# Optimization experiments

Hardware: AMD Instinct MI355X
Metric: run time of the kernel (lower is better)

## Reference

```python
import jax, jax.numpy as jnp
import numpy as np

B, T, C = 2, 2048, 1024
H, M = 16, 64
D = C // H  # head_dim = 64


def setup_inputs() -> dict:
    key = jax.random.key(0)
    ks = jax.random.split(key, 6)
    x = jax.random.normal(ks[0], (B, T, C), dtype=jnp.float32)
    Wqkv = jax.random.normal(ks[1], (3 * C, C), dtype=jnp.float32) / np.sqrt(C)
    bqkv = jax.random.normal(ks[2], (3 * C,), dtype=jnp.float32) * 0.02
    Wout = jax.random.normal(ks[3], (C, C), dtype=jnp.float32) / np.sqrt(C)
    bout = jax.random.normal(ks[4], (C,), dtype=jnp.float32) * 0.02
    proj = jax.random.normal(ks[5], (H, D, M), dtype=jnp.float32) / np.sqrt(D)
    return {"x": x, "Wqkv": Wqkv, "bqkv": bqkv, "Wout": Wout, "bout": bout, "proj": proj}


def reference(x, Wqkv, bqkv, Wout, bout, proj):
    b, t, c = x.shape
    h, d, m = proj.shape
    qkv = x @ Wqkv.T + bqkv                          # [B,T,3C]
    q, k, v = jnp.split(qkv, 3, axis=-1)
    # [B,T,C] -> [B,H,T,D]
    to_heads = lambda z: z.reshape(b, t, h, d).transpose(0, 2, 1, 3)
    q, k, v = to_heads(q), to_heads(k), to_heads(v)
    qf, kf, vf = q.astype(jnp.float32), k.astype(jnp.float32), v.astype(jnp.float32)
    pf = proj.astype(jnp.float32)
    q_prime = jax.nn.relu(jnp.einsum('bhtd,hdm->bhtm', qf, pf))
    k_prime = jax.nn.relu(jnp.einsum('bhtd,hdm->bhtm', kf, pf))
    k_cumsum = jnp.cumsum(k_prime, axis=2)                        # [B,H,T,M]
    kv_prod = jnp.einsum('bhtm,bhtd->bhtmd', k_prime, vf)          # [B,H,T,M,D]
    kv_cumsum = jnp.cumsum(kv_prod, axis=2)                        # [B,H,T,M,D]
    context = jnp.einsum('bhtm,bhtmd->bhtd', q_prime, kv_cumsum)   # [B,H,T,D]
    norm = jnp.einsum('bhtm,bhtm->bht', q_prime, k_cumsum)         # [B,H,T]
    out = context / (norm[..., None] + 1e-6)
    out = out.astype(x.dtype).transpose(0, 2, 1, 3).reshape(b, t, c)
    return out @ Wout.T + bout
```

## Files before the change

### kernel.cpp

```cpp
#include <hip/hip_runtime.h>
#include <cstddef>

#define B_  2
#define T_  2048
#define C_  1024
#define H_  16
#define D_  64
#define M_  64
#define NC_ 32
#define CH_ 64

typedef __attribute__((ext_vector_type(8))) short bf16x8;
typedef __attribute__((ext_vector_type(4))) float f32x4;

__device__ __forceinline__ ushort f2bf(float f) {
    union { float f; unsigned u; } v; v.f = f;
    unsigned r = v.u + 0x7FFF + ((v.u >> 16) & 1);
    return (ushort)(r >> 16);
}
__device__ __forceinline__ float bf2f(ushort u) {
    union { unsigned u; float f; } x; x.u = ((unsigned)u) << 16; return x.f;
}

__device__ __forceinline__ void gld_lds16(const ushort* g, ushort* lds) {
    __builtin_amdgcn_global_load_lds(
        (const __attribute__((address_space(1))) unsigned int*)g,
        (__attribute__((address_space(3))) unsigned int*)lds,
        16, 0, 0);
}

__device__ __forceinline__ bf16x8 frag_ld(const ushort* lds, int row16, int k0, int lane) {
    int r = row16 + (lane & 15);
    int byte = ((k0 * 2) + ((lane >> 4) << 4)) ^ ((r & 7) << 4);
    return *(const bf16x8*)((const char*)lds + r * 128 + byte);
}

#define VMCNT(n) asm volatile("s_waitcnt vmcnt(" #n ")" ::: "memory")
#define BAR() do { __builtin_amdgcn_s_barrier(); __builtin_amdgcn_sched_barrier(0); } while (0)

#define SEG1_ 256
#define SEG2_ 512
#define SEG3_ 1536
#define SEG4_ 1792
#define NPREP_ 1804

__global__ __launch_bounds__(256) void prep_all(
    const float* __restrict__ x, const float* __restrict__ Wqkv,
    const float* __restrict__ bqkv, const float* __restrict__ Wout,
    const float* __restrict__ proj,
    ushort* __restrict__ Wbt, ushort* __restrict__ xbf,
    ushort* __restrict__ WoutBf, float* __restrict__ bbig)
{
    __shared__ float Ws[64 * 128];
    __shared__ float Ps[64 * 64];
    const int blk = blockIdx.x, t = threadIdx.x;
    if (blk < SEG1_) {
        const int sel = blk >> 7, h = (blk >> 3) & 15, cc = blk & 7;
        const int rowbase = sel * 1024 + h * 64;
        {
            const int r0 = t >> 5, cq = t & 31;
#pragma unroll
            for (int k = 0; k < 8; ++k) {
                int r = r0 + 8 * k;
                *(float4*)&Ws[r * 128 + cq * 4] =
                    *(const float4*)&Wqkv[(size_t)(rowbase + r) * 1024 + cc * 128 + cq * 4];
            }
        }
#pragma unroll
        for (int k = 0; k < 4; ++k) {
            int i4 = t + 256 * k;
            *(float4*)&Ps[i4 * 4] = *(const float4*)&proj[h * 4096 + i4 * 4];
        }
        __syncthreads();
#pragma unroll
        for (int k = 0; k < 2; ++k) {
            int id = t + 256 * k;
            int m4 = id >> 5, c4 = id & 31;
            float4 a0 = {0.f,0.f,0.f,0.f}, a1 = a0, a2 = a0, a3 = a0;
            for (int d = 0; d < 64; ++d) {
                float4 w = *(const float4*)&Ws[d * 128 + c4 * 4];
                float4 p = *(const float4*)&Ps[d * 64 + m4 * 4];
                a0.x += p.x*w.x; a0.y += p.x*w.y; a0.z += p.x*w.z; a0.w += p.x*w.w;
                a1.x += p.y*w.x; a1.y += p.y*w.y; a1.z += p.y*w.z; a1.w += p.y*w.w;
                a2.x += p.z*w.x; a2.y += p.z*w.y; a2.z += p.z*w.z; a2.w += p.z*w.w;
                a3.x += p.w*w.x; a3.y += p.w*w.y; a3.z += p.w*w.z; a3.w += p.w*w.w;
            }
            size_t obase = (size_t)(rowbase + m4 * 4) * 1024 + cc * 128 + c4 * 4;
            ushort4 o0 = { f2bf(a0.x), f2bf(a0.y), f2bf(a0.z), f2bf(a0.w) };
            ushort4 o1 = { f2bf(a1.x), f2bf(a1.y), f2bf(a1.z), f2bf(a1.w) };
            ushort4 o2 = { f2bf(a2.x), f2bf(a2.y), f2bf(a2.z), f2bf(a2.w) };
            ushort4 o3 = { f2bf(a3.x), f2bf(a3.y), f2bf(a3.z), f2bf(a3.w) };
            *(ushort4*)&Wbt[obase]          = o0;
            *(ushort4*)&Wbt[obase + 1024]   = o1;
            *(ushort4*)&Wbt[obase + 2048]   = o2;
            *(ushort4*)&Wbt[obase + 3072]   = o3;
        }
    } else if (blk < SEG2_) {
        int bo = blk - SEG1_;
#pragma unroll
        for (int pass = 0; pass < 4; ++pass) {
            int i4 = bo * 1024 + pass * 256 + t;
            float4 v = ((const float4*)Wqkv)[524288 + i4];
            ushort4 o = { f2bf(v.x), f2bf(v.y), f2bf(v.z), f2bf(v.w) };
            ((ushort4*)(Wbt + 2097152))[i4] = o;
        }
    } else if (blk < SEG3_) {
        int bo = blk - SEG2_;
#pragma unroll
        for (int pass = 0; pass < 4; ++pass) {
            int i4 = bo * 1024 + pass * 256 + t;
            float4 v = ((const float4*)x)[i4];
            ushort4 o = { f2bf(v.x), f2bf(v.y), f2bf(v.z), f2bf(v.w) };
            ((ushort4*)xbf)[i4] = o;
        }
    } else if (blk < SEG4_) {
        int bo = blk - SEG3_;
#pragma unroll
        for (int pass = 0; pass < 4; ++pass) {
            int i4 = bo * 1024 + pass * 256 + t;
            float4 v = ((const float4*)Wout)[i4];
            ushort4 o = { f2bf(v.x), f2bf(v.y), f2bf(v.z), f2bf(v.w) };
            ((ushort4*)WoutBf)[i4] = o;
        }
    } else {
        int j = (blk - SEG4_) * 256 + t;
        if (j < 2048) {
            int sel = j >> 10, hm = j & 1023, h = hm >> 6, m = hm & 63;
            const float* b = bqkv + sel * C_ + h * D_;
            const float* p = proj + (size_t)h * D_ * M_ + m;
            float acc = 0.f;
#pragma unroll 8
            for (int d = 0; d < D_; ++d) acc += b[d] * p[(size_t)d * M_];
            bbig[j] = acc;
        } else {
            bbig[j] = bqkv[j];
        }
    }
}

__device__ __forceinline__ void stage_G0(const ushort* __restrict__ Ag, const ushort* __restrict__ Bg,
                                         ushort* Abuf, ushort* Bbuf,
                                         int m0, int n0, int K, int kcol, int w, int lane) {
    const int l8 = lane >> 3, lc = (lane & 7) * 8;
#pragma unroll
    for (int i = 0; i < 4; ++i) {
        int c = w * 4 + i;
        if (c < 8) {
            int fr = (c < 4) ? c * 8 : 64 + (c - 4) * 8;
            int r = fr + l8;
            int cs = lc ^ ((r & 7) << 3);
            gld_lds16(Ag + (size_t)(m0 + r) * K + kcol + cs, Abuf + fr * 64);
        } else {
            int cb = c - 8, g = cb / 6, k8 = cb - g * 6;
            int fr = g * 96 + k8 * 8;
            int r = fr + l8;
            int cs = lc ^ ((r & 7) << 3);
            gld_lds16(Bg + (size_t)(n0 + r) * K + kcol + cs, Bbuf + fr * 64);
        }
    }
}

__device__ __forceinline__ void stage_G1(const ushort* __restrict__ Ag, const ushort* __restrict__ Bg,
                                         ushort* Abuf, ushort* Bbuf,
                                         int m0, int n0, int K, int kcol, int w, int lane) {
    const int l8 = lane >> 3, lc = (lane & 7) * 8;
#pragma unroll
    for (int i = 0; i < 3; ++i) {
        int cb = w * 3 + i, g = cb / 6, k8 = cb - g * 6;
        int fr = g * 96 + 48 + k8 * 8;
        int r = fr + l8;
        int cs = lc ^ ((r & 7) << 3);
        gld_lds16(Bg + (size_t)(n0 + r) * K + kcol + cs, Bbuf + fr * 64);
    }
    {
        int fr = (w < 4) ? 32 + w * 8 : 96 + (w - 4) * 8;
        int r = fr + l8;
        int cs = lc ^ ((r & 7) << 3);
        gld_lds16(Ag + (size_t)(m0 + r) * K + kcol + cs, Abuf + fr * 64);
    }
}

__device__ __forceinline__ void phase_mfma(const ushort* Abuf, const ushort* Bbuf,
                                           f32x4 (&acc)[4][6], int wr, int wc, int lane,
                                           int Mh, int Nh) {
    bf16x8 a[2][2], b[3][2];
#pragma unroll
    for (int i = 0; i < 2; ++i)
#pragma unroll
        for (int ks = 0; ks < 2; ++ks)
            a[i][ks] = frag_ld(Abuf, wr + Mh * 32 + i * 16, ks * 32, lane);
#pragma unroll
    for (int j = 0; j < 3; ++j)
#pragma unroll
        for (int ks = 0; ks < 2; ++ks)
            b[j][ks] = frag_ld(Bbuf, wc + Nh * 48 + j * 16, ks * 32, lane);
    __builtin_amdgcn_s_setprio(1);
#pragma unroll
    for (int ks = 0; ks < 2; ++ks)
#pragma unroll
        for (int i = 0; i < 2; ++i)
#pragma unroll
            for (int j = 0; j < 3; ++j)
                acc[Mh * 2 + i][Nh * 3 + j] = __builtin_amdgcn_mfma_f32_16x16x32_bf16(
                    a[i][ks], b[j][ks], acc[Mh * 2 + i][Nh * 3 + j], 0, 0, 0);
    __builtin_amdgcn_s_setprio(0);
}

__global__ __launch_bounds__(512) void gemm_8phase(
    const ushort* __restrict__ A,
    const ushort* __restrict__ Bt,
    const float* __restrict__ bias,
    ushort* __restrict__ Cout,
    int M, int N, int K, int reluLimit)
{
    __shared__ __align__(16) ushort lds[65536];

    const int tid = threadIdx.x, w = tid >> 6, lane = tid & 63;
    const int m0 = blockIdx.y * 128, n0 = blockIdx.x * 384;
    const int wr = (w >> 2) * 64, wc = (w & 3) * 96;
    f32x4 acc[4][6] = {};
    const int NT = K / 64;

    stage_G0(A, Bt, lds, lds + 16384, m0, n0, K, 0, w, lane);
    stage_G1(A, Bt, lds, lds + 16384, m0, n0, K, 0, w, lane);

    for (int kt = 0; kt < NT - 1; ++kt) {
        const int p = kt & 1;
        ushort* Acur = lds + p * 8192;
        ushort* Anxt = lds + (p ^ 1) * 8192;
        ushort* Bcur = lds + 16384 + p * 24576;
        ushort* Bnxt = lds + 16384 + (p ^ 1) * 24576;
        const int kc1 = (kt + 1) * 64;
        VMCNT(4); BAR();
        stage_G0(A, Bt, Anxt, Bnxt, m0, n0, K, kc1, w, lane);
        phase_mfma(Acur, Bcur, acc, wr, wc, lane, 0, 0);
        VMCNT(5); BAR();
        phase_mfma(Acur, Bcur, acc, wr, wc, lane, 0, 1);
        VMCNT(4); BAR();
        stage_G1(A, Bt, Anxt, Bnxt, m0, n0, K, kc1, w, lane);
        phase_mfma(Acur, Bcur, acc, wr, wc, lane, 1, 0);
        phase_mfma(Acur, Bcur, acc, wr, wc, lane, 1, 1);
    }
    {
        const int p = (NT - 1) & 1;
        ushort* Acur = lds + p * 8192;
        ushort* Bcur = lds + 16384 + p * 24576;
        VMCNT(4); BAR();
        phase_mfma(Acur, Bcur, acc, wr, wc, lane, 0, 0);
        VMCNT(1); BAR();
        phase_mfma(Acur, Bcur, acc, wr, wc, lane, 0, 1);
        VMCNT(0); BAR();
        phase_mfma(Acur, Bcur, acc, wr, wc, lane, 1, 0);
        phase_mfma(Acur, Bcur, acc, wr, wc, lane, 1, 1);
    }

    const int crow = (lane >> 4) * 4, ccol = lane & 15;
#pragma unroll
    for (int nj = 0; nj < 6; ++nj) {
        int col = n0 + wc + nj * 16 + ccol;
        float bv = bias[col];
        bool rl = col < reluLimit;
#pragma unroll
        for (int mi = 0; mi < 4; ++mi) {
#pragma unroll
            for (int rr = 0; rr < 4; ++rr) {
                int row = m0 + wr + mi * 16 + crow + rr;
                float v = acc[mi][nj][rr] + bv;
                if (rl) v = fmaxf(v, 0.f);
                Cout[(size_t)row * N + col] = f2bf(v);
            }
        }
    }
}

__global__ __launch_bounds__(256, 2) void gemm_mfma_bt(
    const ushort* __restrict__ A, const ushort* __restrict__ Bt,
    const float* __restrict__ bias, float* __restrict__ Cmat,
    int M, int N, int K, int reluLimit)
{
    __shared__ __align__(16) ushort As[128 * 32];
    __shared__ __align__(16) ushort Bs[128 * 32];
    const int tid  = threadIdx.x;
    const int wave = tid >> 6, lane = tid & 63;
    const int m0 = blockIdx.y * 128, n0 = blockIdx.x * 128;
    const int wr = (wave >> 1) * 64, wc = (wave & 1) * 64;
    f32x4 acc[4][4] = {};

    const int lrow = lane >> 2;
    const int lcol = (lane & 3) * 8;
    ushort* AsB0 = &As[(wave * 2 + 0) * 512];
    ushort* AsB1 = &As[(wave * 2 + 1) * 512];
    ushort* BsB0 = &Bs[(wave * 2 + 0) * 512];
    ushort* BsB1 = &Bs[(wave * 2 + 1) * 512];
    const ushort* Ag0 = A  + (size_t)(m0 + wave * 32 + lrow) * K + lcol;
    const ushort* Ag1 = Ag0 + (size_t)16 * K;
    const ushort* Bg0 = Bt + (size_t)(n0 + wave * 32 + lrow) * K + lcol;
    const ushort* Bg1 = Bg0 + (size_t)16 * K;

    const int frow = lane & 15, fk = (lane >> 4) * 8;

    for (int k0 = 0; k0 < K; k0 += 32) {
        __syncthreads();
        gld_lds16(Ag0 + k0, AsB0);
        gld_lds16(Ag1 + k0, AsB1);
        gld_lds16(Bg0 + k0, BsB0);
        gld_lds16(Bg1 + k0, BsB1);
        __syncthreads();
        bf16x8 af[4], bfr[4];
#pragma unroll
        for (int i = 0; i < 4; ++i)
            af[i] = *(const bf16x8*)&As[(wr + i * 16 + frow) * 32 + fk];
#pragma unroll
        for (int j = 0; j < 4; ++j)
            bfr[j] = *(const bf16x8*)&Bs[(wc + j * 16 + frow) * 32 + fk];
#pragma unroll
        for (int i = 0; i < 4; ++i)
#pragma unroll
            for (int j = 0; j < 4; ++j)
                acc[i][j] = __builtin_amdgcn_mfma_f32_16x16x32_bf16(af[i], bfr[j], acc[i][j], 0, 0, 0);
    }

    const int crow = (lane >> 4) * 4, ccol = lane & 15;
#pragma unroll
    for (int j = 0; j < 4; ++j) {
        int col = n0 + wc + j * 16 + ccol;
        float bv = bias[col];
        bool rl = col < reluLimit;
#pragma unroll
        for (int i = 0; i < 4; ++i) {
#pragma unroll
            for (int r = 0; r < 4; ++r) {
                int row = m0 + wr + i * 16 + crow + r;
                float v = acc[i][j][r] + bv;
                if (rl) v = fmaxf(v, 0.f);
                Cmat[(size_t)row * N + col] = v;
            }
        }
    }
}

__global__ __launch_bounds__(256) void chunk_kv_mfma(
    const ushort* __restrict__ out1, ushort* __restrict__ VtG,
    float* __restrict__ St, float* __restrict__ sks)
{
    __shared__ unsigned Tl[64 * 76];
    __shared__ ushort Ktb[64 * 64];
    __shared__ ushort Vtb[64 * 64];
    __shared__ float skp[4][64];
    const int blk = blockIdx.x, c = blk & 31, bh = blk >> 5;
    const int b = bh >> 4, h = bh & 15, t0 = c * CH_;
    const int tid = threadIdx.x, wave = tid >> 6, lane = tid & 63;
    const ushort* kg = out1 + (size_t)(b * T_ + t0) * 3072 + C_ + h * D_;
    const ushort* vg = kg + C_;

#pragma unroll
    for (int it = 0; it < 2; ++it) {
        int i = tid + it * 256, r = i >> 3, sl = i & 7;
        bf16x8 v = *(const bf16x8*)(kg + (size_t)r * 3072 + sl * 8);
        unsigned* dst = &Tl[r * 76 + sl * 8];
        uint4 w0 = { (ushort)v[0], (ushort)v[1], (ushort)v[2], (ushort)v[3] };
        uint4 w1 = { (ushort)v[4], (ushort)v[5], (ushort)v[6], (ushort)v[7] };
        *(uint4*)dst = w0;
        *(uint4*)(dst + 4) = w1;
    }
    __syncthreads();
    {
        int m = tid >> 2, tc = tid & 3;
        bf16x8 va, vb;
        float s = 0.f;
#pragma unroll
        for (int k = 0; k < 8; ++k) {
            ushort u = (ushort)Tl[(tc * 16 + k) * 76 + m];
            va[k] = (short)u; s += bf2f(u);
        }
#pragma unroll
        for (int k = 0; k < 8; ++k) {
            ushort u = (ushort)Tl[(tc * 16 + 8 + k) * 76 + m];
            vb[k] = (short)u; s += bf2f(u);
        }
        skp[tc][m] = s;
        int b0 = (tc * 32) ^ ((m & 7) << 4);
        int b1 = (tc * 32 + 16) ^ ((m & 7) << 4);
        *(bf16x8*)((char*)Ktb + m * 128 + b0) = va;
        *(bf16x8*)((char*)Ktb + m * 128 + b1) = vb;
    }
    __syncthreads();
#pragma unroll
    for (int it = 0; it < 2; ++it) {
        int i = tid + it * 256, r = i >> 3, sl = i & 7;
        bf16x8 v = *(const bf16x8*)(vg + (size_t)r * 3072 + sl * 8);
        unsigned* dst = &Tl[r * 76 + sl * 8];
        uint4 w0 = { (ushort)v[0], (ushort)v[1], (ushort)v[2], (ushort)v[3] };
        uint4 w1 = { (ushort)v[4], (ushort)v[5], (ushort)v[6], (ushort)v[7] };
        *(uint4*)dst = w0;
        *(uint4*)(dst + 4) = w1;
    }
    __syncthreads();
    {
        int d = tid >> 2, tc = tid & 3;
        bf16x8 va, vb;
#pragma unroll
        for (int k = 0; k < 8; ++k) va[k] = (short)(ushort)Tl[(tc * 16 + k) * 76 + d];
#pragma unroll
        for (int k = 0; k < 8; ++k) vb[k] = (short)(ushort)Tl[(tc * 16 + 8 + k) * 76 + d];
        int b0 = (tc * 32) ^ ((d & 7) << 4);
        int b1 = (tc * 32 + 16) ^ ((d & 7) << 4);
        *(bf16x8*)((char*)Vtb + d * 128 + b0) = va;
        *(bf16x8*)((char*)Vtb + d * 128 + b1) = vb;
        ushort* og = VtG + (size_t)blk * 4096 + d * 64 + tc * 16;
        *(bf16x8*)og = va;
        *(bf16x8*)(og + 8) = vb;
    }
    __syncthreads();
    const int wr = wave * 16, g = lane >> 4, ccol = lane & 15;
    f32x4 acc[4] = {};
#pragma unroll
    for (int k0 = 0; k0 < 64; k0 += 32) {
        bf16x8 av = frag_ld(Vtb, wr, k0, lane);
#pragma unroll
        for (int j = 0; j < 4; ++j)
            acc[j] = __builtin_amdgcn_mfma_f32_16x16x32_bf16(av, frag_ld(Ktb, j * 16, k0, lane), acc[j], 0, 0, 0);
    }
    float* stg = St + (size_t)blk * 4096;
#pragma unroll
    for (int j = 0; j < 4; ++j)
#pragma unroll
        for (int r = 0; r < 4; ++r)
            stg[(wr + g * 4 + r) * 64 + j * 16 + ccol] = acc[j][r];
    if (tid < 64)
        sks[(size_t)blk * 64 + tid] = skp[0][tid] + skp[1][tid] + skp[2][tid] + skp[3][tid];
}

__global__ __launch_bounds__(256) void chunk_scan2(const float* __restrict__ St,
                                                   const float* __restrict__ sks,
                                                   ushort* __restrict__ Sbf,
                                                   ushort* __restrict__ skb) {
    if (blockIdx.x < 512) {
        int id = blockIdx.x * 256 + threadIdx.x;
        int bh = id >> 12, e = id & 4095;
        const float* p = St + (size_t)bh * NC_ * 4096 + e;
        ushort* q = Sbf + (size_t)bh * NC_ * 4096 + e;
        float run = 0.f;
        for (int c = 0; c < NC_; ++c) {
            q[(size_t)c * 4096] = f2bf(run);
            run += p[(size_t)c * 4096];
        }
    } else {
        int id2 = (blockIdx.x - 512) * 256 + threadIdx.x;
        int bh = id2 >> 6, m = id2 & 63;
        const float* p = sks + (size_t)bh * NC_ * 64 + m;
        ushort* q = skb + (size_t)bh * NC_ * 64 + m;
        float run = 0.f;
        for (int c = 0; c < NC_; ++c) {
            q[c * 64] = f2bf(run);
            run += p[c * 64];
        }
    }
}

__global__ __launch_bounds__(256) void chunk_attn_mfma(
    const ushort* __restrict__ out1, const ushort* __restrict__ VtG,
    const ushort* __restrict__ Sbf, const ushort* __restrict__ skb,
    ushort* __restrict__ attnBf)
{
    __shared__ ushort Ql[64 * 64];
    __shared__ ushort Kl[64 * 64];
    __shared__ ushort Vl[64 * 64];
    __shared__ ushort Al[64 * 64];
    __shared__ ushort Sl[80 * 64];
    const int blk = blockIdx.x, c = blk & 31, bh = blk >> 5;
    const int b = bh >> 4, h = bh & 15, t0 = c * CH_;
    const int tid = threadIdx.x, wave = tid >> 6, lane = tid & 63;
    const ushort* qg  = out1 + (size_t)(b * T_ + t0) * 3072 + h * D_;
    const ushort* kg  = qg + C_;
    const ushort* vtg = VtG + (size_t)blk * 4096;
    const ushort* sbg = Sbf + (size_t)blk * 4096;
#pragma unroll
    for (int it = 0; it < 2; ++it) {
        int i = tid + it * 256, r = i >> 3, sl = i & 7;
        int lo = (sl * 16) ^ ((r & 7) << 4);
        *(bf16x8*)((char*)Ql + r * 128 + lo) = *(const bf16x8*)(qg + (size_t)r * 3072 + sl * 8);
        *(bf16x8*)((char*)Kl + r * 128 + lo) = *(const bf16x8*)(kg + (size_t)r * 3072 + sl * 8);
        *(bf16x8*)((char*)Vl + r * 128 + lo) = *(const bf16x8*)(vtg + r * 64 + sl * 8);
        *(bf16x8*)((char*)Sl + r * 128 + lo) = *(const bf16x8*)(sbg + r * 64 + sl * 8);
    }
    if (tid < 8)
        *(bf16x8*)((char*)Sl + 64 * 128 + tid * 16) = *(const bf16x8*)(skb + (size_t)blk * 64 + tid * 8);
    __syncthreads();

    const int wr = wave * 16, g = lane >> 4, ccol = lane & 15;
    f32x4 accA[4] = {};
#pragma unroll
    for (int k0 = 0; k0 < 64; k0 += 32) {
        bf16x8 aq = frag_ld(Ql, wr, k0, lane);
#pragma unroll
        for (int j = 0; j < 4; ++j)
            accA[j] = __builtin_amdgcn_mfma_f32_16x16x32_bf16(aq, frag_ld(Kl, j * 16, k0, lane), accA[j], 0, 0, 0);
    }
    float rsum[4] = {0.f, 0.f, 0.f, 0.f};
#pragma unroll
    for (int j = 0; j < 4; ++j) {
#pragma unroll
        for (int r = 0; r < 4; ++r) {
            int tl = wr + g * 4 + r, sl2 = j * 16 + ccol;
            float v = (sl2 <= tl) ? accA[j][r] : 0.f;
            rsum[r] += v;
            *(ushort*)((char*)Al + tl * 128 + ((sl2 * 2) ^ ((tl & 7) << 4))) = f2bf(v);
        }
    }
#pragma unroll
    for (int r = 0; r < 4; ++r) {
        rsum[r] += __shfl_xor(rsum[r], 1);
        rsum[r] += __shfl_xor(rsum[r], 2);
        rsum[r] += __shfl_xor(rsum[r], 4);
        rsum[r] += __shfl_xor(rsum[r], 8);
    }
    f32x4 accC[4] = {};
    f32x4 accE = {};
#pragma unroll
    for (int k0 = 0; k0 < 64; k0 += 32) {
        bf16x8 aa = frag_ld(Al, wr, k0, lane);
#pragma unroll
        for (int j = 0; j < 4; ++j)
            accC[j] = __builtin_amdgcn_mfma_f32_16x16x32_bf16(aa, frag_ld(Vl, j * 16, k0, lane), accC[j], 0, 0, 0);
    }
#pragma unroll
    for (int k0 = 0; k0 < 64; k0 += 32) {
        bf16x8 aq = frag_ld(Ql, wr, k0, lane);
#pragma unroll
        for (int j = 0; j < 4; ++j)
            accC[j] = __builtin_amdgcn_mfma_f32_16x16x32_bf16(aq, frag_ld(Sl, j * 16, k0, lane), accC[j], 0, 0, 0);
        accE = __builtin_amdgcn_mfma_f32_16x16x32_bf16(aq, frag_ld(Sl, 64, k0, lane), accE, 0, 0, 0);
    }
    ushort* og = attnBf + (size_t)(b * T_ + t0) * C_ + h * D_;
#pragma unroll
    for (int r = 0; r < 4; ++r) {
        float nq = __shfl(accE[r], (lane & 48));
        float inv = 1.f / (nq + rsum[r] + 1e-6f);
        int tl = wr + g * 4 + r;
#pragma unroll
        for (int j = 0; j < 4; ++j)
            og[(size_t)tl * C_ + j * 16 + ccol] = f2bf(accC[j][r] * inv);
    }
}

extern "C" void kernel_launch(void* const* d_in, const int* in_sizes, int n_in,
                              void* d_out, int out_size, void* d_ws, size_t ws_size,
                              hipStream_t stream) {
    (void)in_sizes; (void)n_in; (void)out_size; (void)ws_size;
    const float* x    = (const float*)d_in[0];
    const float* Wqkv = (const float*)d_in[1];
    const float* bqkv = (const float*)d_in[2];
    const float* Wout = (const float*)d_in[3];
    const float* bout = (const float*)d_in[4];
    const float* proj = (const float*)d_in[5];
    float* out = (float*)d_out;
    char* ws = (char*)d_ws;

    ushort* Wbt    = (ushort*)(ws);
    ushort* xbf    = (ushort*)(ws + (6ull  << 20));
    ushort* WoutBf = (ushort*)(ws + (14ull << 20));
    ushort* attnBf = (ushort*)(ws + (16ull << 20));
    float*  bbig   = (float*) (ws + (24ull << 20));
    ushort* out1   = (ushort*)(ws + (25ull << 20));
    ushort* VtG    = (ushort*)(ws + (49ull << 20));
    float*  St     = (float*) (ws + (57ull << 20));
    ushort* Sbf    = (ushort*)(ws + (73ull << 20));
    float*  sks    = (float*) (ws + (81ull << 20));
    ushort* skb    = (ushort*)(ws + (82ull << 20));

    prep_all<<<NPREP_, 256, 0, stream>>>(x, Wqkv, bqkv, Wout, proj,
                                         Wbt, xbf, WoutBf, bbig);
    gemm_8phase<<<dim3(8, 32), 512, 0, stream>>>(xbf, Wbt, bbig, out1,
                                                 4096, 3072, 1024, 2048);
    chunk_kv_mfma<<<1024, 256, 0, stream>>>(out1, VtG, St, sks);
    chunk_scan2<<<520, 256, 0, stream>>>(St, sks, Sbf, skb);
    chunk_attn_mfma<<<1024, 256, 0, stream>>>(out1, VtG, Sbf, skb, attnBf);
    gemm_mfma_bt<<<dim3(8, 32), 256, 0, stream>>>(attnBf, WoutBf, bout, out,
                                                  4096, 1024, 1024, 0);
}
```

Before: 99.63 us.

## Pipeline output GEMM with 8-phase double-buffered kernel and store chunk states in bf16

Replaces the simple single-buffered output-projection GEMM with a 512-thread, double-buffered, swizzled-LDS, phase-interleaved kernel modeled on the QKV GEMM, so global loads overlap MFMA work. Separately, per-chunk KV state matrices are written as bf16 instead of fp32, which halves the traffic into the scan kernel. The bf16 state storage adds rounding error before the prefix sum, which accumulates over the 32 chunks.

```diff
diff --git a/kernel.cpp b/kernel.cpp
--- a/kernel.cpp
+++ b/kernel.cpp
@@ -207,10 +207,8 @@
 }
 
 __global__ __launch_bounds__(512) void gemm_8phase(
-    const ushort* __restrict__ A,
-    const ushort* __restrict__ Bt,
-    const float* __restrict__ bias,
-    ushort* __restrict__ Cout,
+    const ushort* __restrict__ A, const ushort* __restrict__ Bt,
+    const float* __restrict__ bias, ushort* __restrict__ Cout,
     int M, int N, int K, int reluLimit)
 {
     __shared__ __align__(16) ushort lds[65536];
@@ -273,67 +271,121 @@
     }
 }
 
-__global__ __launch_bounds__(256, 2) void gemm_mfma_bt(
+__device__ __forceinline__ void g2_stage_G0(const ushort* __restrict__ Ag, const ushort* __restrict__ Bg,
+                                            ushort* Abuf, ushort* Bbuf,
+                                            int m0, int n0, int K, int kcol, int w, int lane) {
+    const int l8 = lane >> 3, lc = (lane & 7) * 8;
+    {
+        int rbase = (w < 4) ? w * 8 : 64 + (w - 4) * 8;
+        int r = rbase + l8;
+        int cs = lc ^ ((r & 7) << 3);
+        gld_lds16(Ag + (size_t)(m0 + r) * K + kcol + cs, Abuf + rbase * 64);
+    }
+    {
+        int rbase = (w >> 1) * 32 + (w & 1) * 8;
+        int r = rbase + l8;
+        int cs = lc ^ ((r & 7) << 3);
+        gld_lds16(Bg + (size_t)(n0 + r) * K + kcol + cs, Bbuf + rbase * 64);
+    }
+}
+
+__device__ __forceinline__ void g2_stage_G1(const ushort* __restrict__ Ag, const ushort* __restrict__ Bg,
+                                            ushort* Abuf, ushort* Bbuf,
+                                            int m0, int n0, int K, int kcol, int w, int lane) {
+    const int l8 = lane >> 3, lc = (lane & 7) * 8;
+    {
+        int rbase = 16 + (w >> 1) * 32 + (w & 1) * 8;
+        int r = rbase + l8;
+        int cs = lc ^ ((r & 7) << 3);
+        gld_lds16(Bg + (size_t)(n0 + r) * K + kcol + cs, Bbuf + rbase * 64);
+    }
+    {
+        int rbase = (w < 4) ? 32 + w * 8 : 96 + (w - 4) * 8;
+        int r = rbase + l8;
+        int cs = lc ^ ((r & 7) << 3);
+        gld_lds16(Ag + (size_t)(m0 + r) * K + kcol + cs, Abuf + rbase * 64);
+    }
+}
+
+__device__ __forceinline__ void g2_phase(const ushort* Abuf, const ushort* Bbuf,
+                                         f32x4 (&acc)[4][2], int wr, int wc, int lane,
+                                         int Mh, int Nh) {
+    bf16x8 a[2][2], b[2];
+#pragma unroll
+    for (int i = 0; i < 2; ++i)
+#pragma unroll
+        for (int ks = 0; ks < 2; ++ks)
+            a[i][ks] = frag_ld(Abuf, wr + Mh * 32 + i * 16, ks * 32, lane);
+#pragma unroll
+    for (int ks = 0; ks < 2; ++ks)
+        b[ks] = frag_ld(Bbuf, wc + Nh * 16, ks * 32, lane);
+    __builtin_amdgcn_s_setprio(1);
+#pragma unroll
+    for (int ks = 0; ks < 2; ++ks)
+#pragma unroll
+        for (int i = 0; i < 2; ++i)
+            acc[Mh * 2 + i][Nh] = __builtin_amdgcn_mfma_f32_16x16x32_bf16(
+                a[i][ks], b[ks], acc[Mh * 2 + i][Nh], 0, 0, 0);
+    __builtin_amdgcn_s_setprio(0);
+}
+
+__global__ __launch_bounds__(512, 4) void gemm2_8phase(
     const ushort* __restrict__ A, const ushort* __restrict__ Bt,
-    const float* __restrict__ bias, float* __restrict__ Cmat,
-    int M, int N, int K, int reluLimit)
+    const float* __restrict__ bias, float* __restrict__ Cout,
+    int M, int N, int K)
 {
-    __shared__ __align__(16) ushort As[128 * 32];
-    __shared__ __align__(16) ushort Bs[128 * 32];
-    const int tid  = threadIdx.x;
-    const int wave = tid >> 6, lane = tid & 63;
+    __shared__ __align__(16) ushort lds[32768];
+
+    const int tid = threadIdx.x, w = tid >> 6, lane = tid & 63;
     const int m0 = blockIdx.y * 128, n0 = blockIdx.x * 128;
-    const int wr = (wave >> 1) * 64, wc = (wave & 1) * 64;
-    f32x4 acc[4][4] = {};
-
-    const int lrow = lane >> 2;
-    const int lcol = (lane & 3) * 8;
-    ushort* AsB0 = &As[(wave * 2 + 0) * 512];
-    ushort* AsB1 = &As[(wave * 2 + 1) * 512];
-    ushort* BsB0 = &Bs[(wave * 2 + 0) * 512];
-    ushort* BsB1 = &Bs[(wave * 2 + 1) * 512];
-    const ushort* Ag0 = A  + (size_t)(m0 + wave * 32 + lrow) * K + lcol;
-    const ushort* Ag1 = Ag0 + (size_t)16 * K;
-    const ushort* Bg0 = Bt + (size_t)(n0 + wave * 32 + lrow) * K + lcol;
-    const ushort* Bg1 = Bg0 + (size_t)16 * K;
-
-    const int frow = lane & 15, fk = (lane >> 4) * 8;
-
-    for (int k0 = 0; k0 < K; k0 += 32) {
-        __syncthreads();
-        gld_lds16(Ag0 + k0, AsB0);
-        gld_lds16(Ag1 + k0, AsB1);
-        gld_lds16(Bg0 + k0, BsB0);
-        gld_lds16(Bg1 + k0, BsB1);
-        __syncthreads();
-        bf16x8 af[4], bfr[4];
-#pragma unroll
-        for (int i = 0; i < 4; ++i)
-            af[i] = *(const bf16x8*)&As[(wr + i * 16 + frow) * 32 + fk];
-#pragma unroll
-        for (int j = 0; j < 4; ++j)
-            bfr[j] = *(const bf16x8*)&Bs[(wc + j * 16 + frow) * 32 + fk];
-#pragma unroll
-        for (int i = 0; i < 4; ++i)
-#pragma unroll
-            for (int j = 0; j < 4; ++j)
-                acc[i][j] = __builtin_amdgcn_mfma_f32_16x16x32_bf16(af[i], bfr[j], acc[i][j], 0, 0, 0);
+    const int wr = (w >> 2) * 64, wc = (w & 3) * 32;
+    f32x4 acc[4][2] = {};
+    const int NT = K / 64;
+
+    g2_stage_G0(A, Bt, lds, lds + 16384, m0, n0, K, 0, w, lane);
+    g2_stage_G1(A, Bt, lds, lds + 16384, m0, n0, K, 0, w, lane);
+
+    for (int kt = 0; kt < NT - 1; ++kt) {
+        const int p = kt & 1;
+        ushort* Acur = lds + p * 8192;
+        ushort* Anxt = lds + (p ^ 1) * 8192;
+        ushort* Bcur = lds + 16384 + p * 8192;
+        ushort* Bnxt = lds + 16384 + (p ^ 1) * 8192;
+        const int kc1 = (kt + 1) * 64;
+        VMCNT(2); BAR();
+        g2_stage_G0(A, Bt, Anxt, Bnxt, m0, n0, K, kc1, w, lane);
+        g2_phase(Acur, Bcur, acc, wr, wc, lane, 0, 0);
+        VMCNT(3); BAR();
+        g2_phase(Acur, Bcur, acc, wr, wc, lane, 0, 1);
+        VMCNT(2); BAR();
+        g2_stage_G1(A, Bt, Anxt, Bnxt, m0, n0, K, kc1, w, lane);
+        g2_phase(Acur, Bcur, acc, wr, wc, lane, 1, 0);
+        g2_phase(Acur, Bcur, acc, wr, wc, lane, 1, 1);
+    }
+    {
+        const int p = (NT - 1) & 1;
+        ushort* Acur = lds + p * 8192;
+        ushort* Bcur = lds + 16384 + p * 8192;
+        VMCNT(2); BAR();
+        g2_phase(Acur, Bcur, acc, wr, wc, lane, 0, 0);
+        VMCNT(1); BAR();
+        g2_phase(Acur, Bcur, acc, wr, wc, lane, 0, 1);
+        VMCNT(0); BAR();
+        g2_phase(Acur, Bcur, acc, wr, wc, lane, 1, 0);
+        g2_phase(Acur, Bcur, acc, wr, wc, lane, 1, 1);
     }
 
     const int crow = (lane >> 4) * 4, ccol = lane & 15;
 #pragma unroll
-    for (int j = 0; j < 4; ++j) {
-        int col = n0 + wc + j * 16 + ccol;
+    for (int nj = 0; nj < 2; ++nj) {
+        int col = n0 + wc + nj * 16 + ccol;
         float bv = bias[col];
-        bool rl = col < reluLimit;
-#pragma unroll
-        for (int i = 0; i < 4; ++i) {
-#pragma unroll
-            for (int r = 0; r < 4; ++r) {
-                int row = m0 + wr + i * 16 + crow + r;
-                float v = acc[i][j][r] + bv;
-                if (rl) v = fmaxf(v, 0.f);
-                Cmat[(size_t)row * N + col] = v;
+#pragma unroll
+        for (int mi = 0; mi < 4; ++mi) {
+#pragma unroll
+            for (int rr = 0; rr < 4; ++rr) {
+                int row = m0 + wr + mi * 16 + crow + rr;
+                Cout[(size_t)row * N + col] = acc[mi][nj][rr] + bv;
             }
         }
     }
@@ -341,7 +393,7 @@
 
 __global__ __launch_bounds__(256) void chunk_kv_mfma(
     const ushort* __restrict__ out1, ushort* __restrict__ VtG,
-    float* __restrict__ St, float* __restrict__ sks)
+    ushort* __restrict__ StB, float* __restrict__ sks)
 {
     __shared__ unsigned Tl[64 * 76];
     __shared__ ushort Ktb[64 * 64];
@@ -421,29 +473,29 @@
         for (int j = 0; j < 4; ++j)
             acc[j] = __builtin_amdgcn_mfma_f32_16x16x32_bf16(av, frag_ld(Ktb, j * 16, k0, lane), acc[j], 0, 0, 0);
     }
-    float* stg = St + (size_t)blk * 4096;
+    ushort* stg = StB + (size_t)blk * 4096;
 #pragma unroll
     for (int j = 0; j < 4; ++j)
 #pragma unroll
         for (int r = 0; r < 4; ++r)
-            stg[(wr + g * 4 + r) * 64 + j * 16 + ccol] = acc[j][r];
+            stg[(wr + g * 4 + r) * 64 + j * 16 + ccol] = f2bf(acc[j][r]);
     if (tid < 64)
         sks[(size_t)blk * 64 + tid] = skp[0][tid] + skp[1][tid] + skp[2][tid] + skp[3][tid];
 }
 
-__global__ __launch_bounds__(256) void chunk_scan2(const float* __restrict__ St,
+__global__ __launch_bounds__(256) void chunk_scan2(const ushort* __restrict__ StB,
                                                    const float* __restrict__ sks,
                                                    ushort* __restrict__ Sbf,
                                                    ushort* __restrict__ skb) {
     if (blockIdx.x < 512) {
         int id = blockIdx.x * 256 + threadIdx.x;
         int bh = id >> 12, e = id & 4095;
-        const float* p = St + (size_t)bh * NC_ * 4096 + e;
+        const ushort* p = StB + (size_t)bh * NC_ * 4096 + e;
         ushort* q = Sbf + (size_t)bh * NC_ * 4096 + e;
         float run = 0.f;
         for (int c = 0; c < NC_; ++c) {
             q[(size_t)c * 4096] = f2bf(run);
-            run += p[(size_t)c * 4096];
+            run += bf2f(p[(size_t)c * 4096]);
         }
     } else {
         int id2 = (blockIdx.x - 512) * 256 + threadIdx.x;
@@ -564,18 +616,18 @@
     float*  bbig   = (float*) (ws + (24ull << 20));
     ushort* out1   = (ushort*)(ws + (25ull << 20));
     ushort* VtG    = (ushort*)(ws + (49ull << 20));
-    float*  St     = (float*) (ws + (57ull << 20));
-    ushort* Sbf    = (ushort*)(ws + (73ull << 20));
-    float*  sks    = (float*) (ws + (81ull << 20));
-    ushort* skb    = (ushort*)(ws + (82ull << 20));
+    ushort* StB    = (ushort*)(ws + (57ull << 20));
+    ushort* Sbf    = (ushort*)(ws + (65ull << 20));
+    float*  sks    = (float*) (ws + (73ull << 20));
+    ushort* skb    = (ushort*)(ws + (74ull << 20));
 
     prep_all<<<NPREP_, 256, 0, stream>>>(x, Wqkv, bqkv, Wout, proj,
                                          Wbt, xbf, WoutBf, bbig);
     gemm_8phase<<<dim3(8, 32), 512, 0, stream>>>(xbf, Wbt, bbig, out1,
                                                  4096, 3072, 1024, 2048);
-    chunk_kv_mfma<<<1024, 256, 0, stream>>>(out1, VtG, St, sks);
-    chunk_scan2<<<520, 256, 0, stream>>>(St, sks, Sbf, skb);
+    chunk_kv_mfma<<<1024, 256, 0, stream>>>(out1, VtG, StB, sks);
+    chunk_scan2<<<520, 256, 0, stream>>>(StB, sks, Sbf, skb);
     chunk_attn_mfma<<<1024, 256, 0, stream>>>(out1, VtG, Sbf, skb, attnBf);
-    gemm_mfma_bt<<<dim3(8, 32), 256, 0, stream>>>(attnBf, WoutBf, bout, out,
-                                                  4096, 1024, 1024, 0);
-}
+    gemm2_8phase<<<dim3(8, 32), 512, 0, stream>>>(attnBf, WoutBf, bout, out,
+                                                  4096, 1024, 1024);
+}
```

After: 88.79 us. -10.9%, faster.
